# Kernel tuning notes

Measured on AMD Instinct MI355X. Metric: run time of the kernel, lower is better.

The kernel has to match this reference:

```python
import jax, jax.numpy as jnp
import numpy as np

N_NODES = 50000
N_EDGES = 800000
IN_CH = 128
HID_CH = 128
OUT_CH = 10
NUM_GRAPHS = 128


def setup_inputs() -> dict:
    key = jax.random.key(0)
    ks = jax.random.split(key, 10)
    x = jax.random.normal(ks[0], (N_NODES, IN_CH), dtype=jnp.float32)
    edge_index = jax.random.randint(ks[1], (2, N_EDGES), 0, N_NODES, dtype=jnp.int64)
    batch = jnp.sort(jax.random.randint(ks[2], (N_NODES,), 0, NUM_GRAPHS, dtype=jnp.int64))
    s1 = 1.0 / np.sqrt(IN_CH)
    s2 = 1.0 / np.sqrt(HID_CH)
    W1 = jax.random.uniform(ks[3], (IN_CH, HID_CH), jnp.float32, -s1, s1)
    b1 = jnp.zeros((HID_CH,), jnp.float32)
    W2 = jax.random.uniform(ks[4], (HID_CH, HID_CH), jnp.float32, -s2, s2)
    b2 = jnp.zeros((HID_CH,), jnp.float32)
    Wc = jax.random.uniform(ks[5], (HID_CH, OUT_CH), jnp.float32, -s2, s2)
    bc = jax.random.uniform(ks[6], (OUT_CH,), jnp.float32, -s2, s2)
    return {"x": x, "edge_index": edge_index, "batch": batch,
            "W1": W1, "b1": b1, "W2": W2, "b2": b2, "Wc": Wc, "bc": bc}


def _gcn_norm(edge_index, num_nodes):
    # add self-loops, compute symmetric normalization deg^-1/2[src]*deg^-1/2[dst]
    loop = jnp.arange(num_nodes, dtype=edge_index.dtype)
    src = jnp.concatenate([edge_index[0], loop])
    dst = jnp.concatenate([edge_index[1], loop])
    deg = jax.ops.segment_sum(jnp.ones_like(dst, dtype=jnp.float32), dst,
                              num_segments=num_nodes)
    dinv = jnp.where(deg > 0, jax.lax.rsqrt(deg), 0.0)
    norm = dinv[src] * dinv[dst]
    return src, dst, norm


def _gcn_conv(h, src, dst, norm, W, b, num_nodes):
    h = h @ W                                    # [N, out]
    msg = h[src] * norm[:, None]                 # [E+N, out] gather + scale
    agg = jax.ops.segment_sum(msg, dst, num_segments=num_nodes)
    return agg + b


def reference(x, edge_index, batch, W1, b1, W2, b2, Wc, bc):
    n = x.shape[0]
    src, dst, norm = _gcn_norm(edge_index, n)
    h = jax.nn.relu(_gcn_conv(x, src, dst, norm, W1, b1, n))
    h = jax.nn.relu(_gcn_conv(h, src, dst, norm, W2, b2, n))
    # global mean pool over graphs
    sums = jax.ops.segment_sum(h, batch, num_segments=NUM_GRAPHS)
    cnts = jax.ops.segment_sum(jnp.ones((n,), jnp.float32), batch,
                               num_segments=NUM_GRAPHS)
    pooled = sums / jnp.maximum(cnts, 1.0)[:, None]
    # dropout is identity in eval mode
    return pooled @ Wc + bc
```

## Files before the change

kernel.cpp:

```cpp
#include <hip/hip_runtime.h>

#define N_NODES 50000
#define N_EDGES 800000
#define CH 128
#define NOUT 10
#define NUM_GRAPHS 128
#define SCAN_B 256
#define N_SCAN_BLOCKS ((N_NODES + SCAN_B - 1) / SCAN_B)
#define POOL_CHUNK 50
#define GR 64
#define GEMM_BLOCKS ((N_NODES + GR - 1) / GR)
#define FILL_SEGS 128
#define FILL_CHUNK (N_EDGES / FILL_SEGS)
#define DST_RANGE (N_NODES / 8)

typedef __attribute__((ext_vector_type(8))) short bf16x8;
typedef __attribute__((ext_vector_type(4))) float f32x4;

union FragU { uint4 u; bf16x8 s; };

__device__ __forceinline__ unsigned pack_bf16(float a, float b) {
    unsigned ua = __float_as_uint(a), ub = __float_as_uint(b);
    ua += 0x7fffu + ((ua >> 16) & 1u);
    ub += 0x7fffu + ((ub >> 16) & 1u);
    return (ua >> 16) | (ub & 0xffff0000u);
}

__device__ __forceinline__ unsigned short cvt_bf16(float v) {
    unsigned u = __float_as_uint(v);
    u += 0x7fffu + ((u >> 16) & 1u);
    return (unsigned short)(u >> 16);
}

__global__ __launch_bounds__(256) void k_wcvt(const float* __restrict__ W1,
                                              const float* __restrict__ W2,
                                              unsigned short* __restrict__ Wb1,
                                              unsigned short* __restrict__ Wb2) {
    const float* W = blockIdx.x ? W2 : W1;
    unsigned short* Wb = blockIdx.x ? Wb2 : Wb1;
    for (int i = threadIdx.x; i < CH * CH; i += 256) {
        int k = i >> 7, n = i & 127;
        Wb[((((k >> 3) << 7) + n) << 3) + (k & 7)] = cvt_bf16(W[i]);
    }
}

__device__ __forceinline__ void gemm_body9(const float* __restrict__ X,
                                           const unsigned short* __restrict__ Wb,
                                           unsigned short* __restrict__ Yb,
                                           const float* __restrict__ dinv,
                                           int bid) {
    const int tid = threadIdx.x;
    const int w = tid >> 6;
    const int lane = tid & 63;
    const int m = lane & 15;
    const int quad = lane >> 4;
    const int row0 = bid * GR + w * 16;

    int row_a = row0 + m;
    if (row_a > N_NODES - 1) row_a = N_NODES - 1;
    const float4* Xr = (const float4*)(X + (size_t)row_a * CH) + quad * 2;

    f32x4 acc[8];
    #pragma unroll
    for (int ct = 0; ct < 8; ++ct) acc[ct] = (f32x4){0.f, 0.f, 0.f, 0.f};

    const uint4* Wq = (const uint4*)Wb;
    #pragma unroll
    for (int ks = 0; ks < 4; ++ks) {
        float4 a0 = Xr[ks * 8];
        float4 a1 = Xr[ks * 8 + 1];
        FragU af;
        af.u.x = pack_bf16(a0.x, a0.y);
        af.u.y = pack_bf16(a0.z, a0.w);
        af.u.z = pack_bf16(a1.x, a1.y);
        af.u.w = pack_bf16(a1.z, a1.w);
        const int kg = ks * 4 + quad;
        #pragma unroll
        for (int ct = 0; ct < 8; ++ct) {
            FragU bfu;
            bfu.u = Wq[kg * 128 + ct * 16 + m];
            acc[ct] = __builtin_amdgcn_mfma_f32_16x16x32_bf16(af.s, bfu.s, acc[ct], 0, 0, 0);
        }
    }

    #pragma unroll
    for (int r = 0; r < 4; ++r) {
        int row = row0 + quad * 4 + r;
        if (row < N_NODES) {
            float dv = dinv[row];
            unsigned short* yrow = Yb + (size_t)row * CH + m;
            #pragma unroll
            for (int ct = 0; ct < 8; ++ct)
                yrow[ct * 16] = cvt_bf16(acc[ct][r] * dv);
        }
    }
}

__global__ __launch_bounds__(256) void k_gemm9(const float* __restrict__ X,
                                               const unsigned short* __restrict__ Wb,
                                               unsigned short* __restrict__ Yb,
                                               const float* __restrict__ dinv) {
    gemm_body9(X, Wb, Yb, dinv, blockIdx.x);
}

__global__ __launch_bounds__(256) void k_gemm9b(const float* __restrict__ X,
                                                const unsigned short* __restrict__ Wb,
                                                unsigned short* __restrict__ Yb,
                                                const float* __restrict__ dinv,
                                                float* __restrict__ psum) {
    if (blockIdx.x < 64) psum[blockIdx.x * 256 + threadIdx.x] = 0.f;
    gemm_body9(X, Wb, Yb, dinv, blockIdx.x);
}

__global__ __launch_bounds__(256) void k_hist_x(const int* __restrict__ dst,
                                                int* __restrict__ cnt) {
    const int xcd = blockIdx.x & 7;
    const int seg = blockIdx.x >> 3;
    const int lo = xcd * DST_RANGE, hi = lo + DST_RANGE;
    const int base = seg * FILL_CHUNK;
    for (int it = 0; it < FILL_CHUNK; it += 256) {
        int e = base + it + threadIdx.x;
        if (it + (int)threadIdx.x < FILL_CHUNK) {
            int d = dst[e];
            if (d >= lo && d < hi) atomicAdd(&cnt[d], 1);
        }
    }
}

__global__ __launch_bounds__(SCAN_B) void k_scan1(const int* __restrict__ cnt,
                                                  int* __restrict__ row_start,
                                                  int* __restrict__ bsum) {
    __shared__ int s[SCAN_B];
    int tid = threadIdx.x;
    int i = blockIdx.x * SCAN_B + tid;
    int v = (i < N_NODES) ? cnt[i] : 0;
    s[tid] = v;
    __syncthreads();
    for (int off = 1; off < SCAN_B; off <<= 1) {
        int t = (tid >= off) ? s[tid - off] : 0;
        __syncthreads();
        s[tid] += t;
        __syncthreads();
    }
    if (i < N_NODES) row_start[i] = s[tid] - v;
    if (tid == SCAN_B - 1) bsum[blockIdx.x] = s[tid];
}

__global__ __launch_bounds__(SCAN_B) void k_scan2(int* __restrict__ bsum) {
    __shared__ int s[SCAN_B];
    int tid = threadIdx.x;
    int v = (tid < N_SCAN_BLOCKS) ? bsum[tid] : 0;
    s[tid] = v;
    __syncthreads();
    for (int off = 1; off < SCAN_B; off <<= 1) {
        int t = (tid >= off) ? s[tid - off] : 0;
        __syncthreads();
        s[tid] += t;
        __syncthreads();
    }
    if (tid < N_SCAN_BLOCKS) bsum[tid] = s[tid] - v;
}

__global__ __launch_bounds__(SCAN_B) void k_scan3(int* __restrict__ row_start,
                                                  const int* __restrict__ bsum,
                                                  int* __restrict__ fill_pos,
                                                  const int* __restrict__ cnt,
                                                  float* __restrict__ dinv) {
    int i = blockIdx.x * SCAN_B + threadIdx.x;
    if (i < N_NODES) {
        int rs = row_start[i] + bsum[blockIdx.x];
        row_start[i] = rs;
        fill_pos[i] = rs;
        dinv[i] = rsqrtf((float)(cnt[i] + 1));
    }
}

__global__ __launch_bounds__(256) void k_fill_x(const int* __restrict__ src,
                                                const int* __restrict__ dst,
                                                int* __restrict__ fill_pos,
                                                int* __restrict__ csr_src) {
    const int xcd = blockIdx.x & 7;
    const int seg = blockIdx.x >> 3;
    const int lo = xcd * DST_RANGE, hi = lo + DST_RANGE;
    const int base = seg * FILL_CHUNK;
    for (int it = 0; it < FILL_CHUNK; it += 256) {
        int e = base + it + threadIdx.x;
        if (it + (int)threadIdx.x < FILL_CHUNK) {
            int d = dst[e];
            if (d >= lo && d < hi) {
                int s = src[e];
                int pos = atomicAdd(&fill_pos[d], 1);
                csr_src[pos] = s;
            }
        }
    }
}

__global__ __launch_bounds__(256) void k_gather_bf(const unsigned* __restrict__ tb,
                                                   const int* __restrict__ csr_src,
                                                   const int* __restrict__ row_start,
                                                   const int* __restrict__ cnt,
                                                   const float* __restrict__ dinv,
                                                   const float* __restrict__ b,
                                                   float* __restrict__ h) {
    const int wid = threadIdx.x >> 6;
    const int lane = threadIdx.x & 63;
    const int v = blockIdx.x * 4 + wid;

    const int start = row_start[v];
    const int len = cnt[v];
    const float dv = dinv[v];

    float x0 = 0.f, y0 = 0.f, x1 = 0.f, y1 = 0.f;
    float x2 = 0.f, y2 = 0.f, x3 = 0.f, y3 = 0.f;

    for (int base = 0; base < len; base += 64) {
        int m = len - base; if (m > 64) m = 64;
        int u_l = 0;
        if (lane < m) u_l = csr_src[start + base + lane];
        int j = 0;
        for (; j + 3 < m; j += 4) {
            int u0 = __shfl(u_l, j),     u1 = __shfl(u_l, j + 1);
            int u2 = __shfl(u_l, j + 2), u3 = __shfl(u_l, j + 3);
            unsigned r0 = tb[(size_t)u0 * 64 + lane];
            unsigned r1 = tb[(size_t)u1 * 64 + lane];
            unsigned r2 = tb[(size_t)u2 * 64 + lane];
            unsigned r3 = tb[(size_t)u3 * 64 + lane];
            x0 += __uint_as_float(r0 << 16); y0 += __uint_as_float(r0 & 0xffff0000u);
            x1 += __uint_as_float(r1 << 16); y1 += __uint_as_float(r1 & 0xffff0000u);
            x2 += __uint_as_float(r2 << 16); y2 += __uint_as_float(r2 & 0xffff0000u);
            x3 += __uint_as_float(r3 << 16); y3 += __uint_as_float(r3 & 0xffff0000u);
        }
        for (; j < m; ++j) {
            int u = __shfl(u_l, j);
            unsigned r = tb[(size_t)u * 64 + lane];
            x0 += __uint_as_float(r << 16); y0 += __uint_as_float(r & 0xffff0000u);
        }
    }

    unsigned rs = tb[(size_t)v * 64 + lane];
    float sx = x0 + x1 + x2 + x3 + __uint_as_float(rs << 16);
    float sy = y0 + y1 + y2 + y3 + __uint_as_float(rs & 0xffff0000u);
    float2 bb = ((const float2*)b)[lane];
    float2 o;
    o.x = fmaxf(fmaf(dv, sx, bb.x), 0.f);
    o.y = fmaxf(fmaf(dv, sy, bb.y), 0.f);
    ((float2*)h)[(size_t)v * 64 + lane] = o;
}

__global__ __launch_bounds__(128) void k_pool2(const float* __restrict__ h,
                                               const int* __restrict__ batch,
                                               float* __restrict__ psum) {
    const int c = threadIdx.x;
    const int v0 = blockIdx.x * POOL_CHUNK;
    __shared__ int bg[POOL_CHUNK];
    if (c < POOL_CHUNK) bg[c] = batch[v0 + c];
    __syncthreads();

    float acc = 0.f;
    int g = bg[0];
    #pragma unroll 5
    for (int j = 0; j < POOL_CHUNK; ++j) {
        int bgj = bg[j];
        float val = h[(size_t)(v0 + j) * CH + c];
        if (bgj != g) {
            atomicAdd(&psum[g * CH + c], acc);
            acc = 0.f;
            g = bgj;
        }
        acc += val;
    }
    atomicAdd(&psum[g * CH + c], acc);
}

__global__ __launch_bounds__(128) void k_classify(const float* __restrict__ psum,
                                                  const int* __restrict__ batch,
                                                  const float* __restrict__ Wc,
                                                  const float* __restrict__ bc,
                                                  float* __restrict__ out) {
    __shared__ float p[CH];
    __shared__ float sinv;
    int g = blockIdx.x;
    int tid = threadIdx.x;
    if (tid == 0) {
        int lo = 0, hi = N_NODES;
        while (lo < hi) { int mid = (lo + hi) >> 1; if (batch[mid] < g) lo = mid + 1; else hi = mid; }
        int start = lo;
        lo = 0; hi = N_NODES;
        while (lo < hi) { int mid = (lo + hi) >> 1; if (batch[mid] < g + 1) lo = mid + 1; else hi = mid; }
        sinv = 1.0f / fmaxf((float)(lo - start), 1.0f);
    }
    __syncthreads();
    p[tid] = psum[g * CH + tid] * sinv;
    __syncthreads();
    if (tid < NOUT) {
        float acc = bc[tid];
        #pragma unroll 4
        for (int k = 0; k < CH; ++k) acc += p[k] * Wc[k * NOUT + tid];
        out[g * NOUT + tid] = acc;
    }
}

extern "C" void kernel_launch(void* const* d_in, const int* in_sizes, int n_in,
                              void* d_out, int out_size, void* d_ws, size_t ws_size,
                              hipStream_t stream) {
    const float* x     = (const float*)d_in[0];
    const int*   ei    = (const int*)d_in[1];
    const int*   batch = (const int*)d_in[2];
    const float* W1    = (const float*)d_in[3];
    const float* b1    = (const float*)d_in[4];
    const float* W2    = (const float*)d_in[5];
    const float* b2    = (const float*)d_in[6];
    const float* Wc    = (const float*)d_in[7];
    const float* bc    = (const float*)d_in[8];
    float* out = (float*)d_out;

    const int* src = ei;
    const int* dst = ei + N_EDGES;

    float*          dinv      = (float*)d_ws;
    int*            cnt       = (int*)(dinv + N_NODES);
    int*            row_start = cnt + N_NODES;
    int*            fill_pos  = row_start + N_NODES;
    int*            bsum      = fill_pos + N_NODES;
    int*            csr_src   = bsum + 256;
    unsigned short* wb1       = (unsigned short*)(csr_src + N_EDGES);
    unsigned short* wb2       = wb1 + CH * CH;
    unsigned short* tb        = wb2 + CH * CH;
    float*          hbuf      = (float*)(tb + (size_t)N_NODES * CH);
    float*          psum      = hbuf + (size_t)N_NODES * CH;

    k_wcvt<<<2, 256, 0, stream>>>(W1, W2, wb1, wb2);
    hipMemsetAsync(cnt, 0, N_NODES * sizeof(int), stream);
    k_hist_x<<<FILL_SEGS * 8, 256, 0, stream>>>(dst, cnt);
    k_scan1<<<N_SCAN_BLOCKS, SCAN_B, 0, stream>>>(cnt, row_start, bsum);
    k_scan2<<<1, SCAN_B, 0, stream>>>(bsum);
    k_scan3<<<N_SCAN_BLOCKS, SCAN_B, 0, stream>>>(row_start, bsum, fill_pos, cnt, dinv);
    k_fill_x<<<FILL_SEGS * 8, 256, 0, stream>>>(src, dst, fill_pos, csr_src);

    k_gemm9<<<GEMM_BLOCKS, 256, 0, stream>>>(x, wb1, tb, dinv);
    k_gather_bf<<<N_NODES / 4, 256, 0, stream>>>((unsigned*)tb, csr_src, row_start, cnt, dinv, b1, hbuf);

    k_gemm9b<<<GEMM_BLOCKS, 256, 0, stream>>>(hbuf, wb2, tb, dinv, psum);
    k_gather_bf<<<N_NODES / 4, 256, 0, stream>>>((unsigned*)tb, csr_src, row_start, cnt, dinv, b2, hbuf);

    k_pool2<<<N_NODES / POOL_CHUNK, 128, 0, stream>>>(hbuf, batch, psum);
    k_classify<<<NUM_GRAPHS, 128, 0, stream>>>(psum, batch, Wc, bc, out);
}
```

Before: 300.2 us.

## Fuse cnt zeroing, overlap first GEMM with histogram, defer dinv scaling

Replaces the memset with zeroing blocks inside the weight-conversion kernel. Layer 1's GEMM now runs in the same launch as the degree histogram, writing unscaled bf16 outputs, and dinv is computed inside scan1. The dinv row scaling is then applied in a separate block range of the CSR fill kernel. This removes launches and lets the GEMM overlap the atomic histogram, at the cost of an extra read-modify-write pass over the bf16 feature buffer and a second bf16 rounding step.

Result: faster. 288.3 us (-4.0%).

```diff
diff --git a/kernel.cpp b/kernel.cpp
--- a/kernel.cpp
+++ b/kernel.cpp
@@ -32,18 +32,25 @@
     return (unsigned short)(u >> 16);
 }
 
-__global__ __launch_bounds__(256) void k_wcvt(const float* __restrict__ W1,
+__global__ __launch_bounds__(256) void k_prep(const float* __restrict__ W1,
                                               const float* __restrict__ W2,
                                               unsigned short* __restrict__ Wb1,
-                                              unsigned short* __restrict__ Wb2) {
-    const float* W = blockIdx.x ? W2 : W1;
-    unsigned short* Wb = blockIdx.x ? Wb2 : Wb1;
-    for (int i = threadIdx.x; i < CH * CH; i += 256) {
-        int k = i >> 7, n = i & 127;
-        Wb[((((k >> 3) << 7) + n) << 3) + (k & 7)] = cvt_bf16(W[i]);
-    }
-}
-
+                                              unsigned short* __restrict__ Wb2,
+                                              int* __restrict__ cnt) {
+    if (blockIdx.x < 2) {
+        const float* W = blockIdx.x ? W2 : W1;
+        unsigned short* Wb = blockIdx.x ? Wb2 : Wb1;
+        for (int i = threadIdx.x; i < CH * CH; i += 256) {
+            int k = i >> 7, n = i & 127;
+            Wb[((((k >> 3) << 7) + n) << 3) + (k & 7)] = cvt_bf16(W[i]);
+        }
+    } else {
+        int idx = (blockIdx.x - 2) * 256 + threadIdx.x;
+        if (idx < N_NODES) cnt[idx] = 0;
+    }
+}
+
+template <bool SCALE>
 __device__ __forceinline__ void gemm_body9(const float* __restrict__ X,
                                            const unsigned short* __restrict__ Wb,
                                            unsigned short* __restrict__ Yb,
@@ -87,20 +94,36 @@
     for (int r = 0; r < 4; ++r) {
         int row = row0 + quad * 4 + r;
         if (row < N_NODES) {
-            float dv = dinv[row];
+            float dv = SCALE ? dinv[row] : 1.0f;
             unsigned short* yrow = Yb + (size_t)row * CH + m;
             #pragma unroll
             for (int ct = 0; ct < 8; ++ct)
-                yrow[ct * 16] = cvt_bf16(acc[ct][r] * dv);
-        }
-    }
-}
-
-__global__ __launch_bounds__(256) void k_gemm9(const float* __restrict__ X,
-                                               const unsigned short* __restrict__ Wb,
-                                               unsigned short* __restrict__ Yb,
-                                               const float* __restrict__ dinv) {
-    gemm_body9(X, Wb, Yb, dinv, blockIdx.x);
+                yrow[ct * 16] = cvt_bf16(SCALE ? acc[ct][r] * dv : acc[ct][r]);
+        }
+    }
+}
+
+__global__ __launch_bounds__(256) void k_gemm_hist(const float* __restrict__ X,
+                                                   const unsigned short* __restrict__ Wb,
+                                                   unsigned short* __restrict__ Yb,
+                                                   const int* __restrict__ dst,
+                                                   int* __restrict__ cnt) {
+    if (blockIdx.x < GEMM_BLOCKS) {
+        gemm_body9<false>(X, Wb, Yb, nullptr, blockIdx.x);
+    } else {
+        const int b = blockIdx.x - GEMM_BLOCKS;
+        const int xcd = b & 7;
+        const int seg = b >> 3;
+        const int lo = xcd * DST_RANGE, hi = lo + DST_RANGE;
+        const int base = seg * FILL_CHUNK;
+        for (int it = 0; it < FILL_CHUNK; it += 256) {
+            int e = base + it + threadIdx.x;
+            if (it + (int)threadIdx.x < FILL_CHUNK) {
+                int d = dst[e];
+                if (d >= lo && d < hi) atomicAdd(&cnt[d], 1);
+            }
+        }
+    }
 }
 
 __global__ __launch_bounds__(256) void k_gemm9b(const float* __restrict__ X,
@@ -109,31 +132,18 @@
                                                 const float* __restrict__ dinv,
                                                 float* __restrict__ psum) {
     if (blockIdx.x < 64) psum[blockIdx.x * 256 + threadIdx.x] = 0.f;
-    gemm_body9(X, Wb, Yb, dinv, blockIdx.x);
-}
-
-__global__ __launch_bounds__(256) void k_hist_x(const int* __restrict__ dst,
-                                                int* __restrict__ cnt) {
-    const int xcd = blockIdx.x & 7;
-    const int seg = blockIdx.x >> 3;
-    const int lo = xcd * DST_RANGE, hi = lo + DST_RANGE;
-    const int base = seg * FILL_CHUNK;
-    for (int it = 0; it < FILL_CHUNK; it += 256) {
-        int e = base + it + threadIdx.x;
-        if (it + (int)threadIdx.x < FILL_CHUNK) {
-            int d = dst[e];
-            if (d >= lo && d < hi) atomicAdd(&cnt[d], 1);
-        }
-    }
+    gemm_body9<true>(X, Wb, Yb, dinv, blockIdx.x);
 }
 
 __global__ __launch_bounds__(SCAN_B) void k_scan1(const int* __restrict__ cnt,
                                                   int* __restrict__ row_start,
-                                                  int* __restrict__ bsum) {
+                                                  int* __restrict__ bsum,
+                                                  float* __restrict__ dinv) {
     __shared__ int s[SCAN_B];
     int tid = threadIdx.x;
     int i = blockIdx.x * SCAN_B + tid;
     int v = (i < N_NODES) ? cnt[i] : 0;
+    if (i < N_NODES) dinv[i] = rsqrtf((float)(v + 1));
     s[tid] = v;
     __syncthreads();
     for (int off = 1; off < SCAN_B; off <<= 1) {
@@ -163,35 +173,46 @@
 
 __global__ __launch_bounds__(SCAN_B) void k_scan3(int* __restrict__ row_start,
                                                   const int* __restrict__ bsum,
-                                                  int* __restrict__ fill_pos,
-                                                  const int* __restrict__ cnt,
-                                                  float* __restrict__ dinv) {
+                                                  int* __restrict__ fill_pos) {
     int i = blockIdx.x * SCAN_B + threadIdx.x;
     if (i < N_NODES) {
         int rs = row_start[i] + bsum[blockIdx.x];
         row_start[i] = rs;
         fill_pos[i] = rs;
-        dinv[i] = rsqrtf((float)(cnt[i] + 1));
-    }
-}
-
-__global__ __launch_bounds__(256) void k_fill_x(const int* __restrict__ src,
-                                                const int* __restrict__ dst,
-                                                int* __restrict__ fill_pos,
-                                                int* __restrict__ csr_src) {
-    const int xcd = blockIdx.x & 7;
-    const int seg = blockIdx.x >> 3;
-    const int lo = xcd * DST_RANGE, hi = lo + DST_RANGE;
-    const int base = seg * FILL_CHUNK;
-    for (int it = 0; it < FILL_CHUNK; it += 256) {
-        int e = base + it + threadIdx.x;
-        if (it + (int)threadIdx.x < FILL_CHUNK) {
-            int d = dst[e];
-            if (d >= lo && d < hi) {
-                int s = src[e];
-                int pos = atomicAdd(&fill_pos[d], 1);
-                csr_src[pos] = s;
+    }
+}
+
+__global__ __launch_bounds__(256) void k_fill_scale(const int* __restrict__ src,
+                                                    const int* __restrict__ dst,
+                                                    int* __restrict__ fill_pos,
+                                                    int* __restrict__ csr_src,
+                                                    unsigned* __restrict__ tb32,
+                                                    const float* __restrict__ dinv) {
+    if (blockIdx.x < FILL_SEGS * 8) {
+        const int xcd = blockIdx.x & 7;
+        const int seg = blockIdx.x >> 3;
+        const int lo = xcd * DST_RANGE, hi = lo + DST_RANGE;
+        const int base = seg * FILL_CHUNK;
+        for (int it = 0; it < FILL_CHUNK; it += 256) {
+            int e = base + it + threadIdx.x;
+            if (it + (int)threadIdx.x < FILL_CHUNK) {
+                int d = dst[e];
+                if (d >= lo && d < hi) {
+                    int s = src[e];
+                    int pos = atomicAdd(&fill_pos[d], 1);
+                    csr_src[pos] = s;
+                }
             }
+        }
+    } else {
+        const int wid = (blockIdx.x - FILL_SEGS * 8) * 4 + (threadIdx.x >> 6);
+        const int lane = threadIdx.x & 63;
+        for (int r = wid; r < N_NODES; r += 1024) {
+            float dv = dinv[r];
+            unsigned u = tb32[(size_t)r * 64 + lane];
+            float lo_f = __uint_as_float(u << 16) * dv;
+            float hi_f = __uint_as_float(u & 0xffff0000u) * dv;
+            tb32[(size_t)r * 64 + lane] = pack_bf16(lo_f, hi_f);
         }
     }
 }
@@ -330,15 +351,17 @@
     float*          hbuf      = (float*)(tb + (size_t)N_NODES * CH);
     float*          psum      = hbuf + (size_t)N_NODES * CH;
 
-    k_wcvt<<<2, 256, 0, stream>>>(W1, W2, wb1, wb2);
-    hipMemsetAsync(cnt, 0, N_NODES * sizeof(int), stream);
-    k_hist_x<<<FILL_SEGS * 8, 256, 0, stream>>>(dst, cnt);
-    k_scan1<<<N_SCAN_BLOCKS, SCAN_B, 0, stream>>>(cnt, row_start, bsum);
+    k_prep<<<2 + N_SCAN_BLOCKS, 256, 0, stream>>>(W1, W2, wb1, wb2, cnt);
+
+    k_gemm_hist<<<GEMM_BLOCKS + FILL_SEGS * 8, 256, 0, stream>>>(x, wb1, tb, dst, cnt);
+
+    k_scan1<<<N_SCAN_BLOCKS, SCAN_B, 0, stream>>>(cnt, row_start, bsum, dinv);
     k_scan2<<<1, SCAN_B, 0, stream>>>(bsum);
-    k_scan3<<<N_SCAN_BLOCKS, SCAN_B, 0, stream>>>(row_start, bsum, fill_pos, cnt, dinv);
-    k_fill_x<<<FILL_SEGS * 8, 256, 0, stream>>>(src, dst, fill_pos, csr_src);
-
-    k_gemm9<<<GEMM_BLOCKS, 256, 0, stream>>>(x, wb1, tb, dinv);
+    k_scan3<<<N_SCAN_BLOCKS, SCAN_B, 0, stream>>>(row_start, bsum, fill_pos);
+
+    k_fill_scale<<<FILL_SEGS * 8 + 256, 256, 0, stream>>>(src, dst, fill_pos, csr_src,
+                                                          (unsigned*)tb, dinv);
+
     k_gather_bf<<<N_NODES / 4, 256, 0, stream>>>((unsigned*)tb, csr_src, row_start, cnt, dinv, b1, hbuf);
 
     k_gemm9b<<<GEMM_BLOCKS, 256, 0, stream>>>(hbuf, wb2, tb, dinv, psum);
```
